# Optimization experiments

Hardware: AMD Instinct MI355X
Metric: run time of the kernel (lower is better)

The kernel has to match this reference:

```python
import jax, jax.numpy as jnp
import numpy as np

H = 64   # hidden_size
K = 20   # number of attention groups


def _gru_layer(x, Wih, Whh, bih, bhh):
    # x: [B, T, I] -> [B, T, H]; PyTorch GRU gate order (r, z, n)
    xw = x @ Wih.T + bih  # [B, T, 3H]
    h0 = jnp.zeros((x.shape[0], Whh.shape[1]), x.dtype)

    def step(h, xt):
        gh = h @ Whh.T + bhh
        xr, xz, xn = jnp.split(xt, 3, axis=-1)
        hr, hz, hn = jnp.split(gh, 3, axis=-1)
        r = jax.nn.sigmoid(xr + hr)
        z = jax.nn.sigmoid(xz + hz)
        n = jnp.tanh(xn + r * hn)
        h = (1.0 - z) * n + z * h
        return h, h

    _, hs = jax.lax.scan(step, h0, jnp.swapaxes(xw, 0, 1))
    return jnp.swapaxes(hs, 0, 1)


def setup_inputs():
    key = jax.random.key(0)
    ks = iter(jax.random.split(key, 40))

    def p(shape, fan_in):
        s = 1.0 / np.sqrt(fan_in)
        return jax.random.uniform(next(ks), shape, jnp.float32, -s, s)

    N, T, D = 10240, 60, 6  # N = K * m with m = 512
    inp = {"x": jax.random.normal(next(ks), (N, T, D), jnp.float32)}
    inp.update(
        rnn_Wih0=p((3 * H, D), D), rnn_Whh0=p((3 * H, H), H),
        rnn_bih0=p((3 * H,), H), rnn_bhh0=p((3 * H,), H),
        rnn_Wih1=p((3 * H, H), H), rnn_Whh1=p((3 * H, H), H),
        rnn_bih1=p((3 * H,), H), rnn_bhh1=p((3 * H,), H),
        trans_W=p((H, H), H), trans_b=p((H,), H),
        a=jax.random.normal(next(ks), (2 * H, 1), jnp.float32),
        fc_W=p((H, H), H), fc_b=p((H,), H),
        fco_W=p((1, H), H), fco_b=p((1,), H),
        al_in_W=p((H, H), H), al_in_b=p((H,), H),
        al_Wih0=p((3 * H, H), H), al_Whh0=p((3 * H, H), H),
        al_bih0=p((3 * H,), H), al_bhh0=p((3 * H,), H),
        al_Wih1=p((3 * H, H), H), al_Whh1=p((3 * H, H), H),
        al_bih1=p((3 * H,), H), al_bhh1=p((3 * H,), H),
        al_att1_W=p((H // 2, H), H), al_att1_b=p((H // 2,), H),
        al_att2_W=p((1, H // 2), H // 2),
        al_out_W=p((1, 2 * H), 2 * H), al_out_b=p((1,), 2 * H),
    )
    return inp


def reference(x, rnn_Wih0, rnn_Whh0, rnn_bih0, rnn_bhh0,
              rnn_Wih1, rnn_Whh1, rnn_bih1, rnn_bhh1,
              trans_W, trans_b, a, fc_W, fc_b, fco_W, fco_b,
              al_in_W, al_in_b,
              al_Wih0, al_Whh0, al_bih0, al_bhh0,
              al_Wih1, al_Whh1, al_bih1, al_bhh1,
              al_att1_W, al_att1_b, al_att2_W, al_out_W, al_out_b):
    # ---- 2-layer GRU encoder over time ----
    out = _gru_layer(x, rnn_Wih0, rnn_Whh0, rnn_bih0, rnn_bhh0)
    out = _gru_layer(out, rnn_Wih1, rnn_Whh1, rnn_bih1, rnn_bhh1)
    h = out[:, -1, :].reshape(K, -1, H)  # [K, m, H]

    # ---- dense all-pairs GAT attention (split-projection form of a^T [x_j ; x_i]) ----
    xp = h @ trans_W.T + trans_b         # transformation(x) == transformation(y)
    s_dst = xp @ a[:H, 0]                # contributes along column index j
    s_src = xp @ a[H:, 0]                # contributes along row index i
    score = jax.nn.leaky_relu(s_src[:, :, None] + s_dst[:, None, :])  # [K, m, m]
    att = jax.nn.softmax(score, axis=2)
    h = jnp.einsum('kij,kjd->kid', att, h) + h
    h = h @ fc_W.T + fc_b
    h = jnp.swapaxes(h, 0, 1)            # [m, K, H]  (K acts as seq len for ALSTM)

    # ---- ALSTM (inference: dropout inactive) ----
    z = jnp.tanh(h @ al_in_W.T + al_in_b)
    r = _gru_layer(z, al_Wih0, al_Whh0, al_bih0, al_bhh0)
    r = _gru_layer(r, al_Wih1, al_Whh1, al_bih1, al_bhh1)
    att_s = jax.nn.softmax(jnp.tanh(r @ al_att1_W.T + al_att1_b) @ al_att2_W.T, axis=1)  # [m, K, 1]
    out_att = jnp.sum(r * att_s, axis=1)
    alstm_out = (jnp.concatenate([r[:, -1, :], out_att], axis=1) @ al_out_W.T + al_out_b)[:, 0]

    pred = (jax.nn.leaky_relu(h[:, -1, :]) @ fco_W.T + fco_b)[:, 0]
    return (alstm_out, pred)
```

## Files before the change

### kernel.cpp

```cpp
#include <hip/hip_runtime.h>

#define DEV __device__ __forceinline__

typedef float f2 __attribute__((ext_vector_type(2)));

DEV float fast_rcp(float x) {
#if __has_builtin(__builtin_amdgcn_rcpf)
  return __builtin_amdgcn_rcpf(x);
#else
  return 1.0f / x;
#endif
}
DEV float sigm(float x) { return fast_rcp(1.0f + __expf(-x)); }
DEV float tanh_f(float x) {
  float e = __expf(-2.0f * fabsf(x));
  float t = 1.0f - 2.0f * e * fast_rcp(1.0f + e);
  return copysignf(t, x);
}
DEV float lrelu(float x) { return x > 0.0f ? x : 0.01f * x; }

DEV float wave_sum(float v) {
#pragma unroll
  for (int m = 32; m; m >>= 1) v += __shfl_xor(v, m);
  return v;
}
DEV float wave_max(float v) {
#pragma unroll
  for (int m = 32; m; m >>= 1) v = fmaxf(v, __shfl_xor(v, m));
  return v;
}
DEV float dot4(float4 w, float4 x, float acc) {
  acc = fmaf(w.x, x.x, acc);
  acc = fmaf(w.y, x.y, acc);
  acc = fmaf(w.z, x.z, acc);
  acc = fmaf(w.w, x.w, acc);
  return acc;
}

DEV float bcast(float v, int lane) {
  return __int_as_float(__builtin_amdgcn_readlane(__float_as_int(v), lane));
}

constexpr int E_SPW = 5;
constexpr int E_WAVES = 8;
constexpr int L_W0 = 0;
constexpr int L_W1 = 12288;
constexpr int E_DW = 36864;
constexpr int E_LDS = E_DW * 4;

#define DOT_PHASE(WBASE, HA, AN01, AN23, AN4)                         \
  _Pragma("clang loop unroll_count(4)")                               \
  for (int k = 0; k < 64; ++k) {                                      \
    const int wb = (WBASE) + k * 192 + j3;                            \
    const float wr = lds[wb], wz = lds[wb + 1], wn = lds[wb + 2];     \
    const f2 h01v = {bcast(HA[0], k), bcast(HA[1], k)};               \
    const f2 h23v = {bcast(HA[2], k), bcast(HA[3], k)};               \
    const float h4v = bcast(HA[4], k);                                \
    const f2 wr2 = {wr, wr}, wz2 = {wz, wz}, wn2 = {wn, wn};          \
    ar01 = __builtin_elementwise_fma(wr2, h01v, ar01);                \
    ar23 = __builtin_elementwise_fma(wr2, h23v, ar23);                \
    ar4 = fmaf(wr, h4v, ar4);                                         \
    az01 = __builtin_elementwise_fma(wz2, h01v, az01);                \
    az23 = __builtin_elementwise_fma(wz2, h23v, az23);                \
    az4 = fmaf(wz, h4v, az4);                                         \
    AN01 = __builtin_elementwise_fma(wn2, h01v, AN01);                \
    AN23 = __builtin_elementwise_fma(wn2, h23v, AN23);                \
    AN4 = fmaf(wn, h4v, AN4);                                         \
  }

#define XPART(S, ARx, AZx, ANXx)                       \
  _Pragma("unroll") for (int c = 0; c < 6; ++c) {      \
    const float xk = bcast(xcur, (S) * 6 + c);         \
    ARx = fmaf(wx0[c][0], xk, ARx);                    \
    AZx = fmaf(wx0[c][1], xk, AZx);                    \
    ANXx = fmaf(wx0[c][2], xk, ANXx);                  \
  }

#define EPI(S, ARx, AZx, ANXx, ANHx, HARR, BR, BZ, BXN, BHN)   \
  {                                                            \
    float r_ = sigm((ARx) + (BR));                             \
    float z_ = sigm((AZx) + (BZ));                             \
    float n_ = tanh_f((ANXx) + (BXN) + r_ * ((ANHx) + (BHN))); \
    HARR[S] = (1.0f - z_) * n_ + z_ * HARR[S];                 \
  }

__launch_bounds__(512)
__global__ void gru2_enc(const float* __restrict__ x,
                         const float* __restrict__ w3e0,
                         const float* __restrict__ w3e1,
                         const float* __restrict__ bih0, const float* __restrict__ bhh0,
                         const float* __restrict__ bih1, const float* __restrict__ bhh1,
                         float* __restrict__ h_out) {
  extern __shared__ float lds[];
  const int tid = threadIdx.x;
  const int wave = tid >> 6;
  const int j = tid & 63;
  const int j3 = j * 3;

  {
    const float4* s0 = (const float4*)(w3e0 + 6 * 192);
    for (int i = tid; i < 12288 / 4; i += 512) ((float4*)(lds + L_W0))[i] = s0[i];
    const float4* s1 = (const float4*)w3e1;
    for (int i = tid; i < 24576 / 4; i += 512) ((float4*)(lds + L_W1))[i] = s1[i];
  }
  float wx0[6][3];
#pragma unroll
  for (int k = 0; k < 6; ++k)
#pragma unroll
    for (int g = 0; g < 3; ++g) wx0[k][g] = w3e0[k * 192 + j3 + g];

  const float br0 = bih0[j] + bhh0[j];
  const float bz0 = bih0[64 + j] + bhh0[64 + j];
  const float bxn0 = bih0[128 + j];
  const float bhn0 = bhh0[128 + j];
  const float br1 = bih1[j] + bhh1[j];
  const float bz1 = bih1[64 + j] + bhh1[64 + j];
  const float bxn1 = bih1[128 + j];
  const float bhn1 = bhh1[128 + j];

  float h0r[E_SPW], h1r[E_SPW];
#pragma unroll
  for (int s = 0; s < E_SPW; ++s) { h0r[s] = 0.0f; h1r[s] = 0.0f; }
  __syncthreads();

  const int seq0 = blockIdx.x * (E_WAVES * E_SPW) + wave * E_SPW;
  const int si = j / 6;
  const int ci = j - si * 6;
  const bool xlane = (j < 6 * E_SPW);
  const float* xg = x + (size_t)(seq0 + si) * 360 + ci;

  float xcur = xlane ? xg[0] : 0.0f;

  for (int t = 0; t < 60; ++t) {
    float xnext = (xlane && t + 1 < 60) ? xg[(size_t)(t + 1) * 6] : 0.0f;

    f2 ar01 = {0.f, 0.f}, ar23 = {0.f, 0.f};
    f2 az01 = {0.f, 0.f}, az23 = {0.f, 0.f};
    f2 anx01 = {0.f, 0.f}, anx23 = {0.f, 0.f};
    f2 anh01 = {0.f, 0.f}, anh23 = {0.f, 0.f};
    float ar4 = 0.f, az4 = 0.f, anx4 = 0.f, anh4 = 0.f;

    DOT_PHASE(L_W0, h0r, anh01, anh23, anh4)

    XPART(0, ar01.x, az01.x, anx01.x)
    XPART(1, ar01.y, az01.y, anx01.y)
    XPART(2, ar23.x, az23.x, anx23.x)
    XPART(3, ar23.y, az23.y, anx23.y)
    XPART(4, ar4, az4, anx4)

    EPI(0, ar01.x, az01.x, anx01.x, anh01.x, h0r, br0, bz0, bxn0, bhn0)
    EPI(1, ar01.y, az01.y, anx01.y, anh01.y, h0r, br0, bz0, bxn0, bhn0)
    EPI(2, ar23.x, az23.x, anx23.x, anh23.x, h0r, br0, bz0, bxn0, bhn0)
    EPI(3, ar23.y, az23.y, anx23.y, anh23.y, h0r, br0, bz0, bxn0, bhn0)
    EPI(4, ar4, az4, anx4, anh4, h0r, br0, bz0, bxn0, bhn0)

    ar01 = (f2){0.f, 0.f}; ar23 = (f2){0.f, 0.f};
    az01 = (f2){0.f, 0.f}; az23 = (f2){0.f, 0.f};
    anx01 = (f2){0.f, 0.f}; anx23 = (f2){0.f, 0.f};
    anh01 = (f2){0.f, 0.f}; anh23 = (f2){0.f, 0.f};
    ar4 = 0.f; az4 = 0.f; anx4 = 0.f; anh4 = 0.f;

    DOT_PHASE(L_W1, h0r, anx01, anx23, anx4)
    DOT_PHASE(L_W1 + 64 * 192, h1r, anh01, anh23, anh4)

    EPI(0, ar01.x, az01.x, anx01.x, anh01.x, h1r, br1, bz1, bxn1, bhn1)
    EPI(1, ar01.y, az01.y, anx01.y, anh01.y, h1r, br1, bz1, bxn1, bhn1)
    EPI(2, ar23.x, az23.x, anx23.x, anh23.x, h1r, br1, bz1, bxn1, bhn1)
    EPI(3, ar23.y, az23.y, anx23.y, anh23.y, h1r, br1, bz1, bxn1, bhn1)
    EPI(4, ar4, az4, anx4, anh4, h1r, br1, bz1, bxn1, bhn1)

    xcur = xnext;
  }

#pragma unroll
  for (int s = 0; s < E_SPW; ++s)
    h_out[(size_t)(seq0 + s) * 64 + j] = h1r[s];
}

constexpr int A_W_DW = 128 * 192;
constexpr int A_WAVES = 8;
constexpr int A_LDS = (A_W_DW + A_WAVES * 128) * 4;

__launch_bounds__(512, 2)
__global__ void gru1(const float* __restrict__ xin,
                     const float* __restrict__ w3,
                     const float* __restrict__ bih, const float* __restrict__ bhh,
                     int T,
                     float* __restrict__ rout) {
  extern __shared__ float lds[];
  const int tid = threadIdx.x;
  const int wave = tid >> 6;
  const int j = tid & 63;
  const int j3 = j * 3;
  const int XB = A_W_DW + wave * 128;

  {
    const float4* sp = (const float4*)w3;
    for (int i = tid; i < A_W_DW / 4; i += 512) ((float4*)lds)[i] = sp[i];
  }
  const float br = bih[j] + bhh[j];
  const float bz = bih[64 + j] + bhh[64 + j];
  const float bxn = bih[128 + j];
  const float bhn = bhh[128 + j];

  float hr = 0.0f;
  lds[XB + 64 + j] = 0.0f;
  __syncthreads();

  const int seq = blockIdx.x * A_WAVES + wave;
  const float* xs = xin + (size_t)seq * T * 64;

#define A_QUAD(WROW0, HOFF, AN)                                            \
  {                                                                        \
    float4 hv = *(const float4*)&lds[XB + (HOFF)];                         \
    _Pragma("unroll") for (int c = 0; c < 4; ++c) {                        \
      const float wr = lds[((WROW0) + c) * 192 + j3];                      \
      const float wz = lds[((WROW0) + c) * 192 + j3 + 1];                  \
      const float wn = lds[((WROW0) + c) * 192 + j3 + 2];                  \
      const float hc = (c == 0) ? hv.x : (c == 1) ? hv.y                   \
                      : (c == 2) ? hv.z : hv.w;                            \
      ar = fmaf(wr, hc, ar);                                               \
      az = fmaf(wz, hc, az);                                               \
      AN = fmaf(wn, hc, AN);                                               \
    }                                                                      \
  }

  float xcur = xs[j];
  for (int t = 0; t < T; ++t) {
    float xnext = (t + 1 < T) ? xs[(size_t)(t + 1) * 64 + j] : 0.0f;
    lds[XB + j] = xcur;

    float ar = 0.f, az = 0.f, anx = 0.f, anh = 0.f;
#pragma unroll
    for (int kq = 0; kq < 16; ++kq) A_QUAD(kq * 4, kq * 4, anx);
#pragma unroll
    for (int kq = 0; kq < 16; ++kq) A_QUAD(64 + kq * 4, 64 + kq * 4, anh);

    float r = sigm(ar + br);
    float z = sigm(az + bz);
    float n = tanh_f(anx + bxn + r * (anh + bhn));
    float h = (1.0f - z) * n + z * hr;
    hr = h;
    lds[XB + 64 + j] = h;
    rout[((size_t)seq * T + t) * 64 + j] = h;
    xcur = xnext;
  }
#undef A_QUAD
}

__global__ void w3_prep(const float* __restrict__ Wih0, const float* __restrict__ Whh0,
                        const float* __restrict__ Wih1, const float* __restrict__ Whh1,
                        const float* __restrict__ aWih0, const float* __restrict__ aWhh0,
                        const float* __restrict__ aWih1, const float* __restrict__ aWhh1,
                        float* __restrict__ d_e0, float* __restrict__ d_e1,
                        float* __restrict__ d_a0, float* __restrict__ d_a1) {
  const int sec = blockIdx.x >> 3;
  const int bi = blockIdx.x & 7;
  const float* Wih; const float* Whh; float* dst; int I;
  if (sec == 0)      { Wih = Wih0;  Whh = Whh0;  dst = d_e0; I = 6; }
  else if (sec == 1) { Wih = Wih1;  Whh = Whh1;  dst = d_e1; I = 64; }
  else if (sec == 2) { Wih = aWih0; Whh = aWhh0; dst = d_a0; I = 64; }
  else               { Wih = aWih1; Whh = aWhh1; dst = d_a1; I = 64; }
  const int tot = (I + 64) * 192;
  for (int idx = bi * blockDim.x + threadIdx.x; idx < tot; idx += 8 * blockDim.x) {
    const int k = idx / 192;
    const int rem = idx - k * 192;
    const int jj = rem / 3;
    const int g = rem - jj * 3;
    dst[idx] = (k < I) ? Wih[(g * 64 + jj) * I + k] : Whh[(g * 64 + jj) * 64 + (k - I)];
  }
}

__global__ void gat_prep(const float* __restrict__ tW, const float* __restrict__ tb,
                         const float* __restrict__ a, float* __restrict__ vbuf) {
  const int d = threadIdx.x;
  float vd = 0.0f, vs = 0.0f;
  for (int e = 0; e < 64; ++e) {
    float w = tW[e * 64 + d];
    vd = fmaf(w, a[e], vd);
    vs = fmaf(w, a[64 + e], vs);
  }
  vbuf[d] = vd;
  vbuf[64 + d] = vs;
  if (d == 0) {
    float cd = 0.0f, cs = 0.0f;
    for (int e = 0; e < 64; ++e) {
      cd = fmaf(tb[e], a[e], cd);
      cs = fmaf(tb[e], a[64 + e], cs);
    }
    vbuf[128] = cd;
    vbuf[129] = cs;
  }
}

__global__ void gat_svals(const float* __restrict__ h_enc, const float* __restrict__ vbuf,
                          float* __restrict__ s_src, float* __restrict__ s_dst) {
  const int wave = (blockIdx.x * blockDim.x + threadIdx.x) >> 6;
  const int lane = threadIdx.x & 63;
  float h = h_enc[(size_t)wave * 64 + lane];
  float pd = h * vbuf[lane];
  float ps = h * vbuf[64 + lane];
  pd = wave_sum(pd);
  ps = wave_sum(ps);
  if (lane == 0) {
    s_dst[wave] = pd + vbuf[128];
    s_src[wave] = ps + vbuf[129];
  }
}

__launch_bounds__(256)
__global__ void gat_attn(const float* __restrict__ h_enc,
                         const float* __restrict__ s_src,
                         const float* __restrict__ s_dst,
                         float* __restrict__ hout) {
  const int k = blockIdx.x >> 7;
  const int tile = blockIdx.x & 127;
  const int wv = threadIdx.x >> 6;
  const int lane = threadIdx.x & 63;
  const int i = tile * 4 + wv;
  __shared__ float sdbuf[512];
  __shared__ __align__(16) float pbuf[4][512];

  for (int u = threadIdx.x; u < 512; u += 256) sdbuf[u] = s_dst[k * 512 + u];
  __syncthreads();

  const float si = s_src[k * 512 + i];
  float ev[8];
  float mx = -1e30f;
#pragma unroll
  for (int u = 0; u < 8; ++u) {
    ev[u] = lrelu(si + sdbuf[lane + u * 64]);
    mx = fmaxf(mx, ev[u]);
  }
  mx = wave_max(mx);
  float lsum = 0.0f;
#pragma unroll
  for (int u = 0; u < 8; ++u) {
    float p = __expf(ev[u] - mx);
    pbuf[wv][lane + u * 64] = p;
    lsum += p;
  }
  lsum = wave_sum(lsum);
  const float inv = fast_rcp(lsum);

  const float* hk = h_enc + (size_t)k * 512 * 64;
  const float4* pv = (const float4*)pbuf[wv];
  float acc0 = 0.0f, acc1 = 0.0f;
#pragma unroll 2
  for (int jj = 0; jj < 128; ++jj) {
    float4 p = pv[jj];
    const float* hp = hk + (size_t)(jj * 4) * 64 + lane;
    acc0 = fmaf(p.x, hp[0], acc0);
    acc1 = fmaf(p.y, hp[64], acc1);
    acc0 = fmaf(p.z, hp[128], acc0);
    acc1 = fmaf(p.w, hp[192], acc1);
  }
  hout[((size_t)k * 512 + i) * 64 + lane] =
      (acc0 + acc1) * inv + hk[(size_t)i * 64 + lane];
}

__launch_bounds__(256)
__global__ void gat_out(const float* __restrict__ hin,
                        const float* __restrict__ fcW, const float* __restrict__ fcb,
                        const float* __restrict__ fcoW, const float* __restrict__ fcob,
                        const float* __restrict__ alinW, const float* __restrict__ alinb,
                        float* __restrict__ zout, float* __restrict__ pred) {
  const int wv = threadIdx.x >> 6;
  const int lane = threadIdx.x & 63;
  const int n = blockIdx.x * 4 + wv;
  const int k = n >> 9;
  const int i = n & 511;
  __shared__ __align__(16) float rbuf[4][64];
  __shared__ __align__(16) float rbuf2[4][64];

  float4 fw[16], aw[16];
  {
    const float4* p1 = (const float4*)(fcW + lane * 64);
    const float4* p2 = (const float4*)(alinW + lane * 64);
#pragma unroll
    for (int kk = 0; kk < 16; ++kk) fw[kk] = p1[kk];
#pragma unroll
    for (int kk = 0; kk < 16; ++kk) aw[kk] = p2[kk];
  }

  rbuf[wv][lane] = hin[(size_t)n * 64 + lane];
  float h2 = fcb[lane];
  const float4* rv = (const float4*)rbuf[wv];
#pragma unroll
  for (int kk = 0; kk < 16; ++kk) h2 = dot4(fw[kk], rv[kk], h2);

  if (k == 19) {
    float pv = lrelu(h2) * fcoW[lane];
    pv = wave_sum(pv);
    if (lane == 0) pred[i] = pv + fcob[0];
  }

  rbuf2[wv][lane] = h2;
  float zz = alinb[lane];
  const float4* rv2 = (const float4*)rbuf2[wv];
#pragma unroll
  for (int kk = 0; kk < 16; ++kk) zz = dot4(aw[kk], rv2[kk], zz);
  zout[((size_t)i * 20 + k) * 64 + lane] = tanh_f(zz);
}

__launch_bounds__(256)
__global__ void alstm_head(const float* __restrict__ r1,
                           const float* __restrict__ W1,
                           const float* __restrict__ b1,
                           const float* __restrict__ W2,
                           const float* __restrict__ Wo,
                           const float* __restrict__ bo,
                           float* __restrict__ alstm_out) {
  const int wv = threadIdx.x >> 6;
  const int lane = threadIdx.x & 63;
  const int i = blockIdx.x * 4 + wv;
  const int e = lane & 31;
  __shared__ __align__(16) float rbuf[4][64];
  __shared__ float scb[4][20];

  float4 w1r[16];
  {
    const float4* p = (const float4*)(W1 + e * 64);
#pragma unroll
    for (int kk = 0; kk < 16; ++kk) w1r[kk] = p[kk];
  }
  const float b1e = b1[e];
  const float w2e = W2[e];

  for (int k = 0; k < 20; ++k) {
    rbuf[wv][lane] = r1[((size_t)i * 20 + k) * 64 + lane];
    float u = b1e;
    const float4* rp = (const float4*)rbuf[wv];
#pragma unroll
    for (int kk = 0; kk < 16; ++kk) u = dot4(w1r[kk], rp[kk], u);
    u = tanh_f(u) * w2e;
#pragma unroll
    for (int m = 16; m; m >>= 1) u += __shfl_xor(u, m);
    if (lane == 0) scb[wv][k] = u;
  }

  float mx = -1e30f;
#pragma unroll
  for (int k = 0; k < 20; ++k) mx = fmaxf(mx, scb[wv][k]);
  float p[20];
  float l = 0.0f;
#pragma unroll
  for (int k = 0; k < 20; ++k) {
    p[k] = __expf(scb[wv][k] - mx);
    l += p[k];
  }
  const float inv = fast_rcp(l);

  float oa = 0.0f, rlast = 0.0f;
#pragma unroll
  for (int k = 0; k < 20; ++k) {
    float rv = r1[((size_t)i * 20 + k) * 64 + lane];
    oa = fmaf(p[k], rv, oa);
    if (k == 19) rlast = rv;
  }
  oa *= inv;
  float v = fmaf(Wo[lane], rlast, Wo[64 + lane] * oa);
  v = wave_sum(v);
  if (lane == 0) alstm_out[i] = v + bo[0];
}

extern "C" void kernel_launch(void* const* d_in, const int* in_sizes, int n_in,
                              void* d_out, int out_size, void* d_ws, size_t ws_size,
                              hipStream_t stream) {
  const float* x      = (const float*)d_in[0];
  const float* Wih0   = (const float*)d_in[1];
  const float* Whh0   = (const float*)d_in[2];
  const float* bih0   = (const float*)d_in[3];
  const float* bhh0   = (const float*)d_in[4];
  const float* Wih1   = (const float*)d_in[5];
  const float* Whh1   = (const float*)d_in[6];
  const float* bih1   = (const float*)d_in[7];
  const float* bhh1   = (const float*)d_in[8];
  const float* transW = (const float*)d_in[9];
  const float* transb = (const float*)d_in[10];
  const float* a_vec  = (const float*)d_in[11];
  const float* fcW    = (const float*)d_in[12];
  const float* fcb    = (const float*)d_in[13];
  const float* fcoW   = (const float*)d_in[14];
  const float* fcob   = (const float*)d_in[15];
  const float* alinW  = (const float*)d_in[16];
  const float* alinb  = (const float*)d_in[17];
  const float* aWih0  = (const float*)d_in[18];
  const float* aWhh0  = (const float*)d_in[19];
  const float* abih0  = (const float*)d_in[20];
  const float* abhh0  = (const float*)d_in[21];
  const float* aWih1  = (const float*)d_in[22];
  const float* aWhh1  = (const float*)d_in[23];
  const float* abih1  = (const float*)d_in[24];
  const float* abhh1  = (const float*)d_in[25];
  const float* att1W  = (const float*)d_in[26];
  const float* att1b  = (const float*)d_in[27];
  const float* att2W  = (const float*)d_in[28];
  const float* aloutW = (const float*)d_in[29];
  const float* aloutb = (const float*)d_in[30];

  float* out = (float*)d_out;

  float* W = (float*)d_ws;
  float* h_enc = W; W += 10240 * 64;
  float* vbuf  = W; W += 256;
  float* s_src = W; W += 10240;
  float* s_dst = W; W += 10240;
  float* hout  = W; W += 10240 * 64;
  float* zbuf  = W; W += 512 * 20 * 64;
  float* r1    = W; W += 512 * 20 * 64;
  float* w3a0  = W; W += 24576;
  float* w3a1  = W; W += 24576;
  float* w3e0 = zbuf;
  float* w3e1 = zbuf + 13440;

  static bool attr_done = false;
  if (!attr_done) {
    hipFuncSetAttribute((const void*)gru2_enc,
                        hipFuncAttributeMaxDynamicSharedMemorySize, E_LDS);
    hipFuncSetAttribute((const void*)gru1,
                        hipFuncAttributeMaxDynamicSharedMemorySize, A_LDS);
    attr_done = true;
  }

  w3_prep<<<32, 256, 0, stream>>>(Wih0, Whh0, Wih1, Whh1, aWih0, aWhh0,
                                  aWih1, aWhh1, w3e0, w3e1, w3a0, w3a1);
  gru2_enc<<<256, 512, E_LDS, stream>>>(x, w3e0, w3e1, bih0, bhh0, bih1,
                                        bhh1, h_enc);
  gat_prep<<<1, 64, 0, stream>>>(transW, transb, a_vec, vbuf);
  gat_svals<<<2560, 256, 0, stream>>>(h_enc, vbuf, s_src, s_dst);
  gat_attn<<<2560, 256, 0, stream>>>(h_enc, s_src, s_dst, hout);
  gat_out<<<2560, 256, 0, stream>>>(hout, fcW, fcb, fcoW, fcob, alinW, alinb,
                                    zbuf, out + 512);
  gru1<<<64, 512, A_LDS, stream>>>(zbuf, w3a0, abih0, abhh0, 20, h_enc);
  gru1<<<64, 512, A_LDS, stream>>>(h_enc, w3a1, abih1, abhh1, 20, r1);
  alstm_head<<<128, 256, 0, stream>>>(r1, att1W, att1b, att2W, aloutW, aloutb,
                                      out);
}
```

Measured before the change: 1.385 ms.

## Stage hidden states in per-wave LDS instead of readlane broadcasts in encoder GRU

The encoder GRU dot products used to broadcast each hidden-state element with readlane, which costs scalar-unit work and adds dependency stalls. Each wave now writes its h0/h1 vectors to a private LDS region after every step and reads them back as uniform-address LDS loads inside the dot loops. The last 12 rows of the layer-0 recurrent weights are also held in registers, which shrinks the LDS weight region enough to fit the new hidden-state buffers. In exchange it adds LDS traffic and relies on the wave writing its own LDS data and then reading it without an explicit barrier. Register pressure also rises.

```diff
diff --git a/kernel.cpp b/kernel.cpp
--- a/kernel.cpp
+++ b/kernel.cpp
@@ -44,28 +44,46 @@
 constexpr int E_SPW = 5;
 constexpr int E_WAVES = 8;
 constexpr int L_W0 = 0;
-constexpr int L_W1 = 12288;
-constexpr int E_DW = 36864;
+constexpr int L_W1 = 9984;
+constexpr int L_HB = 34560;
+constexpr int E_DW = 40704;
 constexpr int E_LDS = E_DW * 4;
 
-#define DOT_PHASE(WBASE, HA, AN01, AN23, AN4)                         \
-  _Pragma("clang loop unroll_count(4)")                               \
-  for (int k = 0; k < 64; ++k) {                                      \
-    const int wb = (WBASE) + k * 192 + j3;                            \
-    const float wr = lds[wb], wz = lds[wb + 1], wn = lds[wb + 2];     \
-    const f2 h01v = {bcast(HA[0], k), bcast(HA[1], k)};               \
-    const f2 h23v = {bcast(HA[2], k), bcast(HA[3], k)};               \
-    const float h4v = bcast(HA[4], k);                                \
+#define DOT_ROW(WB, HBASE, K, AN01, AN23, AN4)                        \
+  {                                                                   \
+    const int wb_ = (WB);                                             \
+    const float wr = lds[wb_], wz = lds[wb_ + 1], wn = lds[wb_ + 2];  \
+    const f2 h01 = *(const f2*)&lds[(HBASE) + (K) * 6];               \
+    const f2 h23 = *(const f2*)&lds[(HBASE) + (K) * 6 + 2];           \
+    const float h4 = lds[(HBASE) + (K) * 6 + 4];                      \
     const f2 wr2 = {wr, wr}, wz2 = {wz, wz}, wn2 = {wn, wn};          \
-    ar01 = __builtin_elementwise_fma(wr2, h01v, ar01);                \
-    ar23 = __builtin_elementwise_fma(wr2, h23v, ar23);                \
-    ar4 = fmaf(wr, h4v, ar4);                                         \
-    az01 = __builtin_elementwise_fma(wz2, h01v, az01);                \
-    az23 = __builtin_elementwise_fma(wz2, h23v, az23);                \
-    az4 = fmaf(wz, h4v, az4);                                         \
-    AN01 = __builtin_elementwise_fma(wn2, h01v, AN01);                \
-    AN23 = __builtin_elementwise_fma(wn2, h23v, AN23);                \
-    AN4 = fmaf(wn, h4v, AN4);                                         \
+    ar01 = __builtin_elementwise_fma(wr2, h01, ar01);                 \
+    ar23 = __builtin_elementwise_fma(wr2, h23, ar23);                 \
+    ar4 = fmaf(wr, h4, ar4);                                          \
+    az01 = __builtin_elementwise_fma(wz2, h01, az01);                 \
+    az23 = __builtin_elementwise_fma(wz2, h23, az23);                 \
+    az4 = fmaf(wz, h4, az4);                                          \
+    AN01 = __builtin_elementwise_fma(wn2, h01, AN01);                 \
+    AN23 = __builtin_elementwise_fma(wn2, h23, AN23);                 \
+    AN4 = fmaf(wn, h4, AN4);                                          \
+  }
+
+#define DOT_ROW_REG(WR, WZ, WN, HBASE, K, AN01, AN23, AN4)            \
+  {                                                                   \
+    const float wr = (WR), wz = (WZ), wn = (WN);                      \
+    const f2 h01 = *(const f2*)&lds[(HBASE) + (K) * 6];               \
+    const f2 h23 = *(const f2*)&lds[(HBASE) + (K) * 6 + 2];           \
+    const float h4 = lds[(HBASE) + (K) * 6 + 4];                      \
+    const f2 wr2 = {wr, wr}, wz2 = {wz, wz}, wn2 = {wn, wn};          \
+    ar01 = __builtin_elementwise_fma(wr2, h01, ar01);                 \
+    ar23 = __builtin_elementwise_fma(wr2, h23, ar23);                 \
+    ar4 = fmaf(wr, h4, ar4);                                          \
+    az01 = __builtin_elementwise_fma(wz2, h01, az01);                 \
+    az23 = __builtin_elementwise_fma(wz2, h23, az23);                 \
+    az4 = fmaf(wz, h4, az4);                                          \
+    AN01 = __builtin_elementwise_fma(wn2, h01, AN01);                 \
+    AN23 = __builtin_elementwise_fma(wn2, h23, AN23);                 \
+    AN4 = fmaf(wn, h4, AN4);                                          \
   }
 
 #define XPART(S, ARx, AZx, ANXx)                       \
@@ -96,18 +114,24 @@
   const int wave = tid >> 6;
   const int j = tid & 63;
   const int j3 = j * 3;
+  const int h0base = L_HB + wave * 768;
+  const int h1base = h0base + 384;
 
   {
     const float4* s0 = (const float4*)(w3e0 + 6 * 192);
-    for (int i = tid; i < 12288 / 4; i += 512) ((float4*)(lds + L_W0))[i] = s0[i];
+    for (int i = tid; i < 9984 / 4; i += 512) ((float4*)(lds + L_W0))[i] = s0[i];
     const float4* s1 = (const float4*)w3e1;
     for (int i = tid; i < 24576 / 4; i += 512) ((float4*)(lds + L_W1))[i] = s1[i];
   }
-  float wx0[6][3];
+  float wx0[6][3], wh_hi[12][3];
 #pragma unroll
   for (int k = 0; k < 6; ++k)
 #pragma unroll
     for (int g = 0; g < 3; ++g) wx0[k][g] = w3e0[k * 192 + j3 + g];
+#pragma unroll
+  for (int r = 0; r < 12; ++r)
+#pragma unroll
+    for (int g = 0; g < 3; ++g) wh_hi[r][g] = w3e0[(58 + r) * 192 + j3 + g];
 
   const float br0 = bih0[j] + bhh0[j];
   const float bz0 = bih0[64 + j] + bhh0[64 + j];
@@ -120,7 +144,11 @@
 
   float h0r[E_SPW], h1r[E_SPW];
 #pragma unroll
-  for (int s = 0; s < E_SPW; ++s) { h0r[s] = 0.0f; h1r[s] = 0.0f; }
+  for (int s = 0; s < E_SPW; ++s) {
+    h0r[s] = 0.0f; h1r[s] = 0.0f;
+    lds[h0base + j * 6 + s] = 0.0f;
+    lds[h1base + j * 6 + s] = 0.0f;
+  }
   __syncthreads();
 
   const int seq0 = blockIdx.x * (E_WAVES * E_SPW) + wave * E_SPW;
@@ -140,7 +168,13 @@
     f2 anh01 = {0.f, 0.f}, anh23 = {0.f, 0.f};
     float ar4 = 0.f, az4 = 0.f, anx4 = 0.f, anh4 = 0.f;
 
-    DOT_PHASE(L_W0, h0r, anh01, anh23, anh4)
+#pragma clang loop unroll_count(4)
+    for (int k = 0; k < 52; ++k)
+      DOT_ROW(L_W0 + k * 192 + j3, h0base, k, anh01, anh23, anh4)
+#pragma unroll
+    for (int r = 0; r < 12; ++r)
+      DOT_ROW_REG(wh_hi[r][0], wh_hi[r][1], wh_hi[r][2], h0base, 52 + r,
+                  anh01, anh23, anh4)
 
     XPART(0, ar01.x, az01.x, anx01.x)
     XPART(1, ar01.y, az01.y, anx01.y)
@@ -154,20 +188,40 @@
     EPI(3, ar23.y, az23.y, anx23.y, anh23.y, h0r, br0, bz0, bxn0, bhn0)
     EPI(4, ar4, az4, anx4, anh4, h0r, br0, bz0, bxn0, bhn0)
 
+    {
+      f2 w01 = {h0r[0], h0r[1]};
+      f2 w23 = {h0r[2], h0r[3]};
+      *(f2*)&lds[h0base + j * 6] = w01;
+      *(f2*)&lds[h0base + j * 6 + 2] = w23;
+      lds[h0base + j * 6 + 4] = h0r[4];
+    }
+
     ar01 = (f2){0.f, 0.f}; ar23 = (f2){0.f, 0.f};
     az01 = (f2){0.f, 0.f}; az23 = (f2){0.f, 0.f};
     anx01 = (f2){0.f, 0.f}; anx23 = (f2){0.f, 0.f};
     anh01 = (f2){0.f, 0.f}; anh23 = (f2){0.f, 0.f};
     ar4 = 0.f; az4 = 0.f; anx4 = 0.f; anh4 = 0.f;
 
-    DOT_PHASE(L_W1, h0r, anx01, anx23, anx4)
-    DOT_PHASE(L_W1 + 64 * 192, h1r, anh01, anh23, anh4)
+#pragma clang loop unroll_count(4)
+    for (int k = 0; k < 64; ++k)
+      DOT_ROW(L_W1 + k * 192 + j3, h0base, k, anx01, anx23, anx4)
+#pragma clang loop unroll_count(4)
+    for (int k = 0; k < 64; ++k)
+      DOT_ROW(L_W1 + (64 + k) * 192 + j3, h1base, k, anh01, anh23, anh4)
 
     EPI(0, ar01.x, az01.x, anx01.x, anh01.x, h1r, br1, bz1, bxn1, bhn1)
     EPI(1, ar01.y, az01.y, anx01.y, anh01.y, h1r, br1, bz1, bxn1, bhn1)
     EPI(2, ar23.x, az23.x, anx23.x, anh23.x, h1r, br1, bz1, bxn1, bhn1)
     EPI(3, ar23.y, az23.y, anx23.y, anh23.y, h1r, br1, bz1, bxn1, bhn1)
     EPI(4, ar4, az4, anx4, anh4, h1r, br1, bz1, bxn1, bhn1)
+
+    {
+      f2 w01 = {h1r[0], h1r[1]};
+      f2 w23 = {h1r[2], h1r[3]};
+      *(f2*)&lds[h1base + j * 6] = w01;
+      *(f2*)&lds[h1base + j * 6 + 2] = w23;
+      lds[h1base + j * 6 + 4] = h1r[4];
+    }
 
     xcur = xnext;
   }
```

Measured after the change: 1.367 ms. About the same (-1.3%).
